# Kernel tuning notes

Hardware: AMD Instinct MI355X
Metric: run time of the kernel (lower is better)

The kernel has to match this reference:

```python
import jax, jax.numpy as jnp
import numpy as np

B, S, D, H = 2, 2048, 1024, 16
DK = D // H


def setup_inputs() -> dict:
    key = jax.random.key(0)
    ks = jax.random.split(key, 11)
    inp = {
        'query': jax.random.normal(ks[0], (B, S, D), jnp.float32),
        'key':   jax.random.normal(ks[1], (B, S, D), jnp.float32),
        'value': jax.random.normal(ks[2], (B, S, D), jnp.float32),
        # causal mask, broadcast over heads like mask.unsqueeze(1)
        'mask': jnp.broadcast_to(jnp.tril(jnp.ones((S, S), jnp.int32)), (B, S, S)),
    }
    s = 1.0 / np.sqrt(D)
    for i, nm in enumerate(['q', 'k', 'v', 'o']):
        inp[f'W{nm}'] = jax.random.normal(ks[3 + i], (D, D), jnp.float32) * s
        inp[f'b{nm}'] = jnp.zeros((D,), jnp.float32)
    return inp


def reference(query, key, value, mask, Wq, bq, Wk, bk, Wv, bv, Wo, bo):
    def proj(x, W, b):
        # [B,S,D] -> [B,H,S,DK]
        y = x @ W.T + b
        return y.reshape(B, S, H, DK).transpose(0, 2, 1, 3)

    q = proj(query, Wq, bq)
    k = proj(key, Wk, bk)
    v = proj(value, Wv, bv)

    scores = jnp.einsum('bhsd,bhtd->bhst', q, k) / np.sqrt(DK)
    scores = jnp.where(mask[:, None, :, :] == 0, -1e9, scores)
    p = jax.nn.softmax(scores, axis=-1)  # dropout in eval mode = identity
    x = jnp.einsum('bhst,bhtd->bhsd', p, v)
    x = x.transpose(0, 2, 1, 3).reshape(B, S, D)
    return x @ Wo.T + bo
```

## Files before the change

kernel.cpp:

```cpp
#include <hip/hip_runtime.h>
#include <stdint.h>

#define BB 2
#define SS 2048
#define DD 1024
#define HH 16
#define DKK 64
#define EE 4194304
#define WEE 1048576
#define QSCALE 0.1803368801f

typedef __attribute__((ext_vector_type(8))) short bf16x8;
typedef __attribute__((ext_vector_type(4))) float f32x4;
typedef __attribute__((ext_vector_type(4))) unsigned short u16x4;

__device__ __forceinline__ unsigned short f2bf(float f) {
    union { float f; unsigned int i; } c; c.f = f;
    unsigned int u = c.i;
    return (unsigned short)((u + 0x7FFFu + ((u >> 16) & 1u)) >> 16);
}
__device__ __forceinline__ float bf2f(unsigned short u) {
    union { float f; unsigned int i; } c; c.i = ((unsigned int)u) << 16; return c.f;
}
__device__ __forceinline__ float load1f(const void* p, int idx, int isbf) {
    return isbf ? bf2f(((const unsigned short*)p)[idx]) : ((const float*)p)[idx];
}

#define GLDS16(gp, lp)                                                              \
    __builtin_amdgcn_global_load_lds(                                               \
        (const __attribute__((address_space(1))) void*)(gp),                        \
        (__attribute__((address_space(3))) void*)(lp), 16, 0, 0)

__global__ void detect_dtype_k(const unsigned short* __restrict__ q,
                               int* __restrict__ flag) {
    const int lane = threadIdx.x;
    unsigned short u = q[lane * 2];
    int ex = (u >> 7) & 0xFF;
    bool bad = (ex != 0) && (ex < 110 || ex > 137);
    unsigned long long m = __ballot(bad);
    if (lane == 0) *flag = (__popcll(m) >= 8) ? 0 : 1;
}

__global__ __launch_bounds__(256)
void convert_k(const float* __restrict__ q, const float* __restrict__ k,
               const float* __restrict__ v,
               const float* __restrict__ wq, const float* __restrict__ wk,
               const float* __restrict__ wv, const float* __restrict__ wo,
               unsigned short* __restrict__ Xc, unsigned short* __restrict__ Wc,
               const int* __restrict__ flagp)
{
    if (*flagp) return;
    const size_t e = ((size_t)blockIdx.x * 256 + threadIdx.x) * 8;
    const float* src; unsigned short* dst; size_t off;
    if (e < (size_t)3 * EE) {
        const int t = (int)(e / EE);
        src = (t == 0) ? q : (t == 1) ? k : v;
        off = e - (size_t)t * EE;
        dst = Xc + (size_t)t * EE;
    } else {
        const size_t we = e - (size_t)3 * EE;
        const int t = (int)(we >> 20);
        src = (t == 0) ? wq : (t == 1) ? wk : (t == 2) ? wv : wo;
        off = we & (WEE - 1);
        dst = Wc + (size_t)t * WEE;
    }
    const float4 a = *(const float4*)(src + off);
    const float4 b = *(const float4*)(src + off + 4);
    bf16x8 o;
    o[0] = (short)f2bf(a.x); o[1] = (short)f2bf(a.y);
    o[2] = (short)f2bf(a.z); o[3] = (short)f2bf(a.w);
    o[4] = (short)f2bf(b.x); o[5] = (short)f2bf(b.y);
    o[6] = (short)f2bf(b.z); o[7] = (short)f2bf(b.w);
    *(bf16x8*)(dst + off) = o;
}

__global__ __launch_bounds__(256)
void gemm_qkv(const void* __restrict__ Xq, const void* __restrict__ Xk,
              const void* __restrict__ Xv,
              const void* __restrict__ Wqp, const void* __restrict__ Wkp,
              const void* __restrict__ Wvp,
              const void* __restrict__ bqp, const void* __restrict__ bkp,
              const void* __restrict__ bvp,
              const unsigned short* __restrict__ Xc,
              const unsigned short* __restrict__ Wc,
              unsigned short* __restrict__ qb, unsigned short* __restrict__ kb,
              unsigned short* __restrict__ vtb, const int* __restrict__ flagp)
{
    const int isbf = *flagp;
    const int z = blockIdx.z;
    const unsigned short* Xg = isbf
        ? (const unsigned short*)((z == 0) ? Xq : (z == 1) ? Xk : Xv)
        : Xc + (size_t)z * EE;
    const unsigned short* Wg = isbf
        ? (const unsigned short*)((z == 0) ? Wqp : (z == 1) ? Wkp : Wvp)
        : Wc + (size_t)z * WEE;
    const void* bias = (z == 0) ? bqp : (z == 1) ? bkp : bvp;

    __shared__ __align__(16) unsigned short As[3][128 * 32];
    __shared__ __align__(16) unsigned short Bs[3][128 * 32];

    const int tid  = threadIdx.x;
    const int lane = tid & 63, w = tid >> 6;
    const int l15  = lane & 15, quad = lane >> 4;
    const int wr = (w >> 1) * 64, wc = (w & 1) * 64;
    const int r0 = blockIdx.x * 128, c0 = blockIdx.y * 128;
    const int srow = tid >> 2;
    const int scol = (((tid & 3) ^ ((tid >> 3) & 3)) << 3);
    const int rdo  = ((quad ^ ((l15 >> 1) & 3)) << 3);

    const unsigned short* xp0 = Xg + (size_t)(r0 + srow) * DD + scol;
    const unsigned short* xp1 = Xg + (size_t)(r0 + 64 + srow) * DD + scol;
    const unsigned short* wp0 = Wg + (size_t)(c0 + srow) * DD + scol;
    const unsigned short* wp1 = Wg + (size_t)(c0 + 64 + srow) * DD + scol;

#define STAGE_G(buf, kk)                                                       \
    do {                                                                       \
        GLDS16(xp0 + (kk), &As[buf][tid * 8]);                                 \
        GLDS16(xp1 + (kk), &As[buf][2048 + tid * 8]);                          \
        GLDS16(wp0 + (kk), &Bs[buf][tid * 8]);                                 \
        GLDS16(wp1 + (kk), &Bs[buf][2048 + tid * 8]);                          \
    } while (0)

#define LOADFRAG_G(buf)                                                        \
    do {                                                                       \
        _Pragma("unroll")                                                      \
        for (int mi = 0; mi < 4; ++mi)                                         \
            af[mi] = *(const bf16x8*)(&As[buf][(wr + mi * 16 + l15) * 32 +     \
                                               rdo]);                          \
        _Pragma("unroll")                                                      \
        for (int ni = 0; ni < 4; ++ni)                                         \
            bfr[ni] = *(const bf16x8*)(&Bs[buf][(wc + ni * 16 + l15) * 32 +    \
                                                rdo]);                         \
    } while (0)

#define MFMA_G()                                                               \
    do {                                                                       \
        __builtin_amdgcn_s_setprio(1);                                         \
        _Pragma("unroll")                                                      \
        for (int mi = 0; mi < 4; ++mi)                                         \
            _Pragma("unroll")                                                  \
            for (int ni = 0; ni < 4; ++ni)                                     \
                acc[mi][ni] = __builtin_amdgcn_mfma_f32_16x16x32_bf16(         \
                    af[mi], bfr[ni], acc[mi][ni], 0, 0, 0);                    \
        __builtin_amdgcn_s_setprio(0);                                         \
    } while (0)

#define PHASE_G(cb, nb, kn)                                                    \
    do {                                                                       \
        asm volatile("s_waitcnt vmcnt(4)" ::: "memory");                       \
        __builtin_amdgcn_s_barrier();                                          \
        __builtin_amdgcn_sched_barrier(0);                                     \
        LOADFRAG_G(cb);                                                        \
        STAGE_G(nb, kn);                                                       \
        __builtin_amdgcn_sched_barrier(0);                                     \
        MFMA_G();                                                              \
    } while (0)

    f32x4 acc[4][4] = {};
    bf16x8 af[4], bfr[4];

    STAGE_G(0, 0);
    STAGE_G(1, 32);
    for (int s = 0; s < 30; s += 3) {
        const int k0 = s * 32;
        PHASE_G(0, 2, k0 + 64);
        PHASE_G(1, 0, k0 + 96);
        PHASE_G(2, 1, k0 + 128);
    }
    asm volatile("s_waitcnt vmcnt(4)" ::: "memory");
    __builtin_amdgcn_s_barrier();
    __builtin_amdgcn_sched_barrier(0);
    LOADFRAG_G(0);
    MFMA_G();
    asm volatile("s_waitcnt vmcnt(0)" ::: "memory");
    __builtin_amdgcn_s_barrier();
    __builtin_amdgcn_sched_barrier(0);
    LOADFRAG_G(1);
    MFMA_G();

#pragma unroll
    for (int mi = 0; mi < 4; ++mi) {
#pragma unroll
        for (int ni = 0; ni < 4; ++ni) {
            const int col = c0 + wc + ni * 16 + l15;
            const float bv = load1f(bias, col, isbf);
            const int h = col >> 6, dk = col & 63;
            const int m0 = r0 + wr + mi * 16 + quad * 4;
            const int bb = m0 >> 11, s0 = m0 & (SS - 1);
            const int bh = bb * HH + h;
            if (z == 0) {
#pragma unroll
                for (int r = 0; r < 4; ++r)
                    qb[((size_t)bh * SS + s0 + r) * DKK + dk] =
                        f2bf((acc[mi][ni][r] + bv) * QSCALE);
            } else if (z == 1) {
#pragma unroll
                for (int r = 0; r < 4; ++r) {
                    const int t = s0 + r;
                    kb[((((size_t)bh * 128 + (t >> 4)) * 8 + (dk >> 3)) * 16 +
                        (t & 15)) * 8 + (dk & 7)] = f2bf(acc[mi][ni][r] + bv);
                }
            } else {
                u16x4 pv;
#pragma unroll
                for (int r = 0; r < 4; ++r) pv[r] = f2bf(acc[mi][ni][r] + bv);
                const int t = s0;
                *(u16x4*)&vtb[((((size_t)bh * 64 + (t >> 5)) * 4 + (dk >> 4)) * 64 +
                               ((t >> 3) & 3) * 16 + (dk & 15)) * 8 + (t & 7)] = pv;
            }
        }
    }
#undef STAGE_G
#undef LOADFRAG_G
#undef MFMA_G
#undef PHASE_G
}

template <bool MASKED>
__device__ __forceinline__ void attn_tile(
    const int t0, const int q0, const int l15, const int quad,
    const unsigned short* __restrict__ Kb, const unsigned short* __restrict__ Vb,
    const bf16x8 (&qf)[2], f32x4 (&Oa)[4], float (&ls)[4],
    unsigned short* __restrict__ Pw)
{
    bf16x8 kf[4][2];
#pragma unroll
    for (int ni = 0; ni < 4; ++ni)
#pragma unroll
        for (int ks = 0; ks < 2; ++ks)
            kf[ni][ks] = *(const bf16x8*)(Kb +
                ((size_t)(((t0 >> 4) + ni) * 8 + ks * 4 + quad) * 16 + l15) * 8);

    f32x4 sc[4] = {};
    __builtin_amdgcn_s_setprio(1);
#pragma unroll
    for (int ks = 0; ks < 2; ++ks)
#pragma unroll
        for (int ni = 0; ni < 4; ++ni)
            sc[ni] = __builtin_amdgcn_mfma_f32_16x16x32_bf16(
                qf[ks], kf[ni][ks], sc[ni], 0, 0, 0);
    __builtin_amdgcn_s_setprio(0);

    bf16x8 vf[4][2];
#pragma unroll
    for (int nd = 0; nd < 4; ++nd)
#pragma unroll
        for (int ks = 0; ks < 2; ++ks)
            vf[nd][ks] = *(const bf16x8*)(Vb +
                ((size_t)(((t0 >> 5) + ks) * 4 + nd) * 64 + quad * 16 + l15) * 8);

#pragma unroll
    for (int ni = 0; ni < 4; ++ni)
#pragma unroll
        for (int r = 0; r < 4; ++r) {
            float s = sc[ni][r];
            if (MASKED && (t0 + ni * 16 + l15 > q0 + quad * 4 + r))
                s = -__builtin_inff();
            const float p = __builtin_amdgcn_exp2f(s);
            const unsigned int pu = __float_as_uint(p);
            ls[r] += __uint_as_float(pu & 0xFFFF0000u);
            Pw[(quad * 4 + r) * 72 + ni * 16 + l15] = (unsigned short)(pu >> 16);
        }

    bf16x8 pf[2];
#pragma unroll
    for (int ks = 0; ks < 2; ++ks)
        pf[ks] = *(const bf16x8*)(Pw + l15 * 72 + ks * 32 + quad * 8);
    __builtin_amdgcn_s_setprio(1);
#pragma unroll
    for (int ks = 0; ks < 2; ++ks)
#pragma unroll
        for (int nd = 0; nd < 4; ++nd)
            Oa[nd] = __builtin_amdgcn_mfma_f32_16x16x32_bf16(
                pf[ks], vf[nd][ks], Oa[nd], 0, 0, 0);
    __builtin_amdgcn_s_setprio(0);
}

__global__ __launch_bounds__(256)
void attn_mfma(const unsigned short* __restrict__ Qg,
               const unsigned short* __restrict__ Kf,
               const unsigned short* __restrict__ Vf,
               unsigned short* __restrict__ Og)
{
    __shared__ __align__(16) unsigned short Ps[4][16 * 72];
    const int tid  = threadIdx.x;
    const int lane = tid & 63, w = tid >> 6;
    const int l15 = lane & 15, quad = lane >> 4;
    const int bh = blockIdx.x;
    const int qt = (gridDim.y - 1 - blockIdx.y) * 4 + w;
    const int q0 = qt * 16;
    unsigned short* Pw = &Ps[w][0];

    const unsigned short* Qb = Qg + (size_t)bh * SS * DKK;
    const unsigned short* Kb = Kf + (size_t)bh * SS * DKK;
    const unsigned short* Vb = Vf + (size_t)bh * SS * DKK;

    bf16x8 qf[2];
#pragma unroll
    for (int ks = 0; ks < 2; ++ks)
        qf[ks] = *(const bf16x8*)(Qb + (size_t)(q0 + l15) * DKK + ks * 32 + quad * 8);

    f32x4 Oa[4] = {};
    float ls[4] = {};
    const int nfull = q0 >> 6;

    for (int tt = 0; tt < nfull; ++tt)
        attn_tile<false>(tt * 64, q0, l15, quad, Kb, Vb, qf, Oa, ls, Pw);
    attn_tile<true>(nfull * 64, q0, l15, quad, Kb, Vb, qf, Oa, ls, Pw);

    const int bb = bh >> 4, h = bh & (HH - 1);
#pragma unroll
    for (int r = 0; r < 4; ++r) {
        float l = ls[r];
        l += __shfl_xor(l, 1);
        l += __shfl_xor(l, 2);
        l += __shfl_xor(l, 4);
        l += __shfl_xor(l, 8);
        const float inv = 1.0f / l;
        const int s = q0 + quad * 4 + r;
#pragma unroll
        for (int nd = 0; nd < 4; ++nd)
            Og[((size_t)bb * SS + s) * DD + h * 64 + nd * 16 + l15] =
                f2bf(Oa[nd][r] * inv);
    }
}

__global__ __launch_bounds__(256)
void gemm_out(const unsigned short* __restrict__ Xa, const void* __restrict__ W,
              const unsigned short* __restrict__ Wcs,
              const void* __restrict__ bias, void* __restrict__ Y,
              const int* __restrict__ flagp)
{
    const int isbf = *flagp;
    const unsigned short* Wg = isbf ? (const unsigned short*)W : Wcs;

    __shared__ __align__(16) unsigned short As[3][64 * 32];
    __shared__ __align__(16) unsigned short Bs[3][128 * 32];

    const int tid  = threadIdx.x;
    const int lane = tid & 63, w = tid >> 6;
    const int l15  = lane & 15, quad = lane >> 4;
    const int wr = (w >> 1) * 32, wc = (w & 1) * 64;
    const int r0 = blockIdx.x * 64, c0 = blockIdx.y * 128;
    const int srow = tid >> 2;
    const int scol = (((tid & 3) ^ ((tid >> 3) & 3)) << 3);
    const int rdo  = ((quad ^ ((l15 >> 1) & 3)) << 3);

    const unsigned short* xp0 = Xa + (size_t)(r0 + srow) * DD + scol;
    const unsigned short* wp0 = Wg + (size_t)(c0 + srow) * DD + scol;
    const unsigned short* wp1 = Wg + (size_t)(c0 + 64 + srow) * DD + scol;

#define STAGE_O(buf, kk)                                                       \
    do {                                                                       \
        GLDS16(xp0 + (kk), &As[buf][tid * 8]);                                 \
        GLDS16(wp0 + (kk), &Bs[buf][tid * 8]);                                 \
        GLDS16(wp1 + (kk), &Bs[buf][2048 + tid * 8]);                          \
    } while (0)

#define LOADFRAG_O(buf)                                                        \
    do {                                                                       \
        _Pragma("unroll")                                                      \
        for (int mi = 0; mi < 2; ++mi)                                         \
            af[mi] = *(const bf16x8*)(&As[buf][(wr + mi * 16 + l15) * 32 +     \
                                               rdo]);                          \
        _Pragma("unroll")                                                      \
        for (int ni = 0; ni < 4; ++ni)                                         \
            bfr[ni] = *(const bf16x8*)(&Bs[buf][(wc + ni * 16 + l15) * 32 +    \
                                                rdo]);                         \
    } while (0)

#define MFMA_O()                                                               \
    do {                                                                       \
        __builtin_amdgcn_s_setprio(1);                                         \
        _Pragma("unroll")                                                      \
        for (int mi = 0; mi < 2; ++mi)                                         \
            _Pragma("unroll")                                                  \
            for (int ni = 0; ni < 4; ++ni)                                     \
                acc[mi][ni] = __builtin_amdgcn_mfma_f32_16x16x32_bf16(         \
                    af[mi], bfr[ni], acc[mi][ni], 0, 0, 0);                    \
        __builtin_amdgcn_s_setprio(0);                                         \
    } while (0)

#define PHASE_O(cb, nb, kn)                                                    \
    do {                                                                       \
        asm volatile("s_waitcnt vmcnt(3)" ::: "memory");                       \
        __builtin_amdgcn_s_barrier();                                          \
        __builtin_amdgcn_sched_barrier(0);                                     \
        LOADFRAG_O(cb);                                                        \
        STAGE_O(nb, kn);                                                       \
        __builtin_amdgcn_sched_barrier(0);                                     \
        MFMA_O();                                                              \
    } while (0)

    f32x4 acc[2][4] = {};
    bf16x8 af[2], bfr[4];

    STAGE_O(0, 0);
    STAGE_O(1, 32);
    for (int s = 0; s < 30; s += 3) {
        const int k0 = s * 32;
        PHASE_O(0, 2, k0 + 64);
        PHASE_O(1, 0, k0 + 96);
        PHASE_O(2, 1, k0 + 128);
    }
    asm volatile("s_waitcnt vmcnt(3)" ::: "memory");
    __builtin_amdgcn_s_barrier();
    __builtin_amdgcn_sched_barrier(0);
    LOADFRAG_O(0);
    MFMA_O();
    asm volatile("s_waitcnt vmcnt(0)" ::: "memory");
    __builtin_amdgcn_s_barrier();
    __builtin_amdgcn_sched_barrier(0);
    LOADFRAG_O(1);
    MFMA_O();

#pragma unroll
    for (int mi = 0; mi < 2; ++mi) {
#pragma unroll
        for (int ni = 0; ni < 4; ++ni) {
            const int col = c0 + wc + ni * 16 + l15;
            const float bv = load1f(bias, col, isbf);
            const int m0 = r0 + wr + mi * 16 + quad * 4;
#pragma unroll
            for (int r = 0; r < 4; ++r) {
                const float val = acc[mi][ni][r] + bv;
                if (isbf) ((unsigned short*)Y)[(size_t)(m0 + r) * DD + col] = f2bf(val);
                else      ((float*)Y)[(size_t)(m0 + r) * DD + col] = val;
            }
        }
    }
#undef STAGE_O
#undef LOADFRAG_O
#undef MFMA_O
#undef PHASE_O
}

extern "C" void kernel_launch(void* const* d_in, const int* in_sizes, int n_in,
                              void* d_out, int out_size, void* d_ws, size_t ws_size,
                              hipStream_t stream)
{
    const void* query = d_in[0];
    const void* key   = d_in[1];
    const void* value = d_in[2];
    const void* Wq = d_in[4];  const void* bq = d_in[5];
    const void* Wk = d_in[6];  const void* bk = d_in[7];
    const void* Wv = d_in[8];  const void* bv = d_in[9];
    const void* Wo = d_in[10]; const void* bo = d_in[11];

    int* flag = (int*)d_ws;
    unsigned short* base = (unsigned short*)((char*)d_ws + 256);
    const size_t E = EE;
    unsigned short* qb  = base;
    unsigned short* kb  = base + E;
    unsigned short* vtb = base + 2 * E;
    unsigned short* Wc  = base + 3 * E;
    unsigned short* Xc  = base + 4 * E;
    unsigned short* ab  = Xc;

    detect_dtype_k<<<1, 64, 0, stream>>>((const unsigned short*)query, flag);
    convert_k<<<8192, 256, 0, stream>>>((const float*)query, (const float*)key,
                                        (const float*)value, (const float*)Wq,
                                        (const float*)Wk, (const float*)Wv,
                                        (const float*)Wo, Xc, Wc, flag);
    gemm_qkv<<<dim3(32, 8, 3), 256, 0, stream>>>(query, key, value, Wq, Wk, Wv,
                                                 bq, bk, bv, Xc, Wc,
                                                 qb, kb, vtb, flag);
    attn_mfma<<<dim3(32, 32), 256, 0, stream>>>(qb, kb, vtb, ab);
    gemm_out<<<dim3(64, 8), 256, 0, stream>>>(ab, Wo, Wc + 3 * (size_t)WEE, bo,
                                              d_out, flag);
}
```

Before: 233.7 us.

## Stage K/V tiles through double-buffered LDS shared across the block's waves

Each 64-key K/V tile is now loaded once per block into double-buffered shared memory with direct global-to-LDS loads, and all four waves read fragments from LDS. Before, every wave fetched the same K/V fragments from global memory on its own. The next tile is prefetched while the current one is computed, so load latency overlaps with MFMA work. In exchange the waves must stay in lockstep through barriers, and per-block LDS use grows, which may limit occupancy.

After: 231.3 us, median of 2. About the same (-1.0%).

```diff
diff --git a/kernel.cpp b/kernel.cpp
--- a/kernel.cpp
+++ b/kernel.cpp
@@ -217,9 +217,9 @@
 }
 
 template <bool MASKED>
-__device__ __forceinline__ void attn_tile(
+__device__ __forceinline__ void attn_tile_lds(
     const int t0, const int q0, const int l15, const int quad,
-    const unsigned short* __restrict__ Kb, const unsigned short* __restrict__ Vb,
+    const unsigned short* Kl, const unsigned short* Vl,
     const bf16x8 (&qf)[2], f32x4 (&Oa)[4], float (&ls)[4],
     unsigned short* __restrict__ Pw)
 {
@@ -228,8 +228,8 @@
     for (int ni = 0; ni < 4; ++ni)
 #pragma unroll
         for (int ks = 0; ks < 2; ++ks)
-            kf[ni][ks] = *(const bf16x8*)(Kb +
-                ((size_t)(((t0 >> 4) + ni) * 8 + ks * 4 + quad) * 16 + l15) * 8);
+            kf[ni][ks] = *(const bf16x8*)(Kl +
+                (((ni * 8 + ks * 4 + quad) * 16 + l15) * 8));
 
     f32x4 sc[4] = {};
     __builtin_amdgcn_s_setprio(1);
@@ -246,8 +246,8 @@
     for (int nd = 0; nd < 4; ++nd)
 #pragma unroll
         for (int ks = 0; ks < 2; ++ks)
-            vf[nd][ks] = *(const bf16x8*)(Vb +
-                ((size_t)(((t0 >> 5) + ks) * 4 + nd) * 64 + quad * 16 + l15) * 8);
+            vf[nd][ks] = *(const bf16x8*)(Vl +
+                (((ks * 4 + nd) * 64 + quad * 16 + l15) * 8));
 
 #pragma unroll
     for (int ni = 0; ni < 4; ++ni)
@@ -282,12 +282,15 @@
                const unsigned short* __restrict__ Vf,
                unsigned short* __restrict__ Og)
 {
+    __shared__ __align__(16) unsigned short Ks[2][4096];
+    __shared__ __align__(16) unsigned short Vs[2][4096];
     __shared__ __align__(16) unsigned short Ps[4][16 * 72];
     const int tid  = threadIdx.x;
     const int lane = tid & 63, w = tid >> 6;
     const int l15 = lane & 15, quad = lane >> 4;
     const int bh = blockIdx.x;
-    const int qt = (gridDim.y - 1 - blockIdx.y) * 4 + w;
+    const int g = gridDim.y - 1 - blockIdx.y;
+    const int qt = g * 4 + w;
     const int q0 = qt * 16;
     unsigned short* Pw = &Ps[w][0];
 
@@ -295,6 +298,14 @@
     const unsigned short* Kb = Kf + (size_t)bh * SS * DKK;
     const unsigned short* Vb = Vf + (size_t)bh * SS * DKK;
 
+#define STAGE_T(buf, tt)                                                       \
+    do {                                                                       \
+        GLDS16(Kb + (size_t)(tt) * 4096 + tid * 8,        &Ks[buf][tid * 8]);  \
+        GLDS16(Kb + (size_t)(tt) * 4096 + 2048 + tid * 8, &Ks[buf][2048 + tid * 8]); \
+        GLDS16(Vb + (size_t)(tt) * 4096 + tid * 8,        &Vs[buf][tid * 8]);  \
+        GLDS16(Vb + (size_t)(tt) * 4096 + 2048 + tid * 8, &Vs[buf][2048 + tid * 8]); \
+    } while (0)
+
     bf16x8 qf[2];
 #pragma unroll
     for (int ks = 0; ks < 2; ++ks)
@@ -302,11 +313,25 @@
 
     f32x4 Oa[4] = {};
     float ls[4] = {};
-    const int nfull = q0 >> 6;
-
-    for (int tt = 0; tt < nfull; ++tt)
-        attn_tile<false>(tt * 64, q0, l15, quad, Kb, Vb, qf, Oa, ls, Pw);
-    attn_tile<true>(nfull * 64, q0, l15, quad, Kb, Vb, qf, Oa, ls, Pw);
+
+    STAGE_T(0, 0);
+    int cur = 0;
+    for (int tt = 0; tt < g; ++tt) {
+        STAGE_T(cur ^ 1, tt + 1);
+        asm volatile("s_waitcnt vmcnt(4)" ::: "memory");
+        __builtin_amdgcn_s_barrier();
+        __builtin_amdgcn_sched_barrier(0);
+        attn_tile_lds<false>(tt * 64, q0, l15, quad,
+                             &Ks[cur][0], &Vs[cur][0], qf, Oa, ls, Pw);
+        __builtin_amdgcn_s_barrier();
+        cur ^= 1;
+    }
+    asm volatile("s_waitcnt vmcnt(0)" ::: "memory");
+    __builtin_amdgcn_s_barrier();
+    __builtin_amdgcn_sched_barrier(0);
+    attn_tile_lds<true>(g * 64, q0, l15, quad,
+                        &Ks[cur][0], &Vs[cur][0], qf, Oa, ls, Pw);
+#undef STAGE_T
 
     const int bb = bh >> 4, h = bh & (HH - 1);
 #pragma unroll
```
